# Kernel optimization log

Measured on AMD Instinct MI355X. Metric: run time of the kernel, lower is better.

## Reference

```python
import jax, jax.numpy as jnp
import numpy as np

EMB_K = 512
EMB_DIM = 256
BETA = 0.25
GAMMA = 0.99
EPS = 1e-5
B, T = 16, 4096


def setup_inputs() -> dict:
    key = jax.random.key(0)
    k1, k2, k3 = jax.random.split(key, 3)
    return {
        "inputs": jax.random.normal(k1, (B, EMB_DIM, T), dtype=jnp.float32),
        "emb_weight": jax.random.normal(k2, (EMB_K, EMB_DIM), dtype=jnp.float32),
        "ema_w": jax.random.normal(k3, (EMB_K, EMB_DIM), dtype=jnp.float32),
        "ema_cluster_size": jnp.zeros((EMB_K,), dtype=jnp.float32),
    }


def reference(inputs, emb_weight, ema_w, ema_cluster_size):
    # [B, D, T] -> [B, T, D]
    x = jnp.transpose(inputs, (0, 2, 1))
    flat = x.reshape(-1, EMB_DIM)  # [N, D]

    # squared euclidean distances to codebook: [N, K]
    dist = (jnp.sum(flat * flat, axis=1, keepdims=True)
            + jnp.sum(emb_weight * emb_weight, axis=1)
            - 2.0 * flat @ emb_weight.T)
    idx = jnp.argmin(dist, axis=1)            # [N]
    enc = jax.nn.one_hot(idx, EMB_K, dtype=flat.dtype)  # [N, K]

    # --- EMA codebook update (training branch) ---
    counts = jax.ops.segment_sum(jnp.ones_like(idx, dtype=flat.dtype), idx,
                                 num_segments=EMB_K)  # == enc.sum(0)
    new_cs = ema_cluster_size * GAMMA + (1.0 - GAMMA) * counts
    n = jnp.sum(new_cs)
    new_cs = (new_cs + EPS) / (n + EMB_K * EPS) * n
    dw = jax.ops.segment_sum(flat, idx, num_segments=EMB_K)  # == enc.T @ flat
    new_ema_w = ema_w * GAMMA + (1.0 - GAMMA) * dw
    new_emb_weight = new_ema_w / new_cs[:, None]

    # quantize with updated codebook (gather == enc @ new_emb_weight)
    Q = new_emb_weight[idx].reshape(x.shape)  # [B, T, D]

    e_latent_loss = jnp.mean((jax.lax.stop_gradient(Q) - x) ** 2)
    loss = BETA * e_latent_loss

    # straight-through
    Q_st = x + jax.lax.stop_gradient(Q - x)

    avg_probs = jnp.mean(enc, axis=0)
    PP = jnp.exp(-jnp.sum(avg_probs * jnp.log(avg_probs + 1e-10)))

    return loss, jnp.transpose(Q_st, (0, 2, 1)), PP, enc
```

## Files before the change

kernel.cpp:

```cpp
#include <hip/hip_runtime.h>

#define N_TOT 65536
#define DIM 256
#define KK 512
#define TT 4096
#define BB 16

typedef short bf16x8 __attribute__((ext_vector_type(8)));
typedef float f32x4 __attribute__((ext_vector_type(4)));

__device__ __forceinline__ ushort f2bf(float f) {
    unsigned u = __float_as_uint(f);
    unsigned r = (u + 0x7fffu + ((u >> 16) & 1u)) >> 16;
    return (ushort)r;
}

__global__ void k_se(const float* __restrict__ emb, float* __restrict__ se) {
    int wid = threadIdx.x >> 6, lane = threadIdx.x & 63;
    int k = blockIdx.x * 4 + wid;
    const float4* e4 = (const float4*)emb;
    float4 v = e4[k * 64 + lane];
    float s = v.x * v.x + v.y * v.y + v.z * v.z + v.w * v.w;
#pragma unroll
    for (int m = 1; m < 64; m <<= 1) s += __shfl_xor(s, m);
    if (lane == 0) se[k] = s;
}

__global__ void k_split_e(const float* __restrict__ emb, ushort* __restrict__ eb) {
    int k = blockIdx.x, tid = threadIdx.x;
    int c0 = tid * 4;
    float4 v = *(const float4*)(emb + k * DIM + c0);
    float f[4] = {v.x, v.y, v.z, v.w};
    ushort h[4], l[4];
#pragma unroll
    for (int j = 0; j < 4; ++j) {
        h[j] = f2bf(f[j]);
        float hf = __uint_as_float(((unsigned)h[j]) << 16);
        l[j] = f2bf(f[j] - hf);
    }
    uint2 hp = make_uint2((unsigned)h[0] | ((unsigned)h[1] << 16),
                          (unsigned)h[2] | ((unsigned)h[3] << 16));
    uint2 lp = make_uint2((unsigned)l[0] | ((unsigned)l[1] << 16),
                          (unsigned)l[2] | ((unsigned)l[3] << 16));
    *(uint2*)(eb + (size_t)k * 512 + c0) = hp;
    *(uint2*)(eb + (size_t)k * 512 + 256 + c0) = lp;
}

__global__ __launch_bounds__(256) void k_split_x(const float* __restrict__ in,
                                                 ushort* __restrict__ xt) {
    __shared__ float ls[64][65];
    int tid = threadIdx.x;
    int b = blockIdx.x >> 8;
    int rest = blockIdx.x & 255;
    int tt = rest >> 2, dt = rest & 3;
    int t0 = tt * 64, d0 = dt * 64;
    int tl = tid & 63, dg = tid >> 6;
    const float* src = in + (size_t)b * DIM * TT + t0 + tl;
#pragma unroll
    for (int p = 0; p < 16; ++p) {
        int d = dg * 16 + p;
        ls[d][tl] = src[(size_t)(d0 + d) * TT];
    }
    __syncthreads();
    int c0 = dg * 16;
    int n = b * TT + t0 + tl;
    ushort* row = xt + (size_t)n * 512;
    ushort h[16], l[16];
#pragma unroll
    for (int j = 0; j < 16; ++j) {
        float v = ls[c0 + j][tl];
        h[j] = f2bf(v);
        float hf = __uint_as_float(((unsigned)h[j]) << 16);
        l[j] = f2bf(v - hf);
    }
    uint hu[8], lu[8];
#pragma unroll
    for (int j = 0; j < 8; ++j) {
        hu[j] = (unsigned)h[2 * j] | ((unsigned)h[2 * j + 1] << 16);
        lu[j] = (unsigned)l[2 * j] | ((unsigned)l[2 * j + 1] << 16);
    }
    *(uint4*)(row + d0 + c0) = make_uint4(hu[0], hu[1], hu[2], hu[3]);
    *(uint4*)(row + d0 + c0 + 8) = make_uint4(hu[4], hu[5], hu[6], hu[7]);
    *(uint4*)(row + 256 + d0 + c0) = make_uint4(lu[0], lu[1], lu[2], lu[3]);
    *(uint4*)(row + 256 + d0 + c0 + 8) = make_uint4(lu[4], lu[5], lu[6], lu[7]);
}

__global__ void k_zero(float* __restrict__ dw, unsigned* __restrict__ counts,
                       unsigned* __restrict__ lossd) {
    int i = blockIdx.x * 256 + threadIdx.x;
    if (i < 131072) dw[i] = 0.f;
    int j = i - 131072;
    if (j >= 0 && j < 512) counts[j] = 0u;
    if (j >= 512 && j < 514) lossd[j - 512] = 0u;
}

__global__ __launch_bounds__(256) void k_dist(
    const ushort* __restrict__ xt, const ushort* __restrict__ eb,
    const float* __restrict__ se,
    float* __restrict__ partd, int* __restrict__ parti) {
    __shared__ ushort As[128 * 64];
    __shared__ ushort Bs[128 * 64];
    const int tid = threadIdx.x;
    const int lane = tid & 63, w = tid >> 6;
    const int bj = blockIdx.x, bi = blockIdx.y;
    const int n0 = bi * 128, k0 = bj * 128;
    const int wr = w >> 1, wc = w & 1;

    f32x4 acc[4][4] = {};

    for (int it = 0; it < 12; ++it) {
        const int region = it >> 2, sub = it & 3;
        const int aoff = (region == 2 ? 256 : 0) + sub * 64;
        const int boff = (region == 1 ? 256 : 0) + sub * 64;
#pragma unroll
        for (int i = 0; i < 4; ++i) {
            int r = i * 32 + w * 8 + (lane >> 3);
            int slot = (lane & 7) ^ (r & 7);
            const ushort* ga = xt + (size_t)(n0 + r) * 512 + aoff + slot * 8;
            const ushort* gb = eb + (size_t)(k0 + r) * 512 + boff + slot * 8;
            __builtin_amdgcn_global_load_lds(
                (const __attribute__((address_space(1))) void*)ga,
                (__attribute__((address_space(3))) void*)&As[(size_t)(i * 256 + w * 64) * 8],
                16, 0, 0);
            __builtin_amdgcn_global_load_lds(
                (const __attribute__((address_space(1))) void*)gb,
                (__attribute__((address_space(3))) void*)&Bs[(size_t)(i * 256 + w * 64) * 8],
                16, 0, 0);
        }
        __syncthreads();
#pragma unroll
        for (int kk = 0; kk < 2; ++kk) {
            bf16x8 af[4], bfr[4];
#pragma unroll
            for (int mi = 0; mi < 4; ++mi) {
                int row = wr * 64 + mi * 16 + (lane & 15);
                int slot = (kk * 4 + (lane >> 4)) ^ (row & 7);
                af[mi] = *(const bf16x8*)&As[row * 64 + slot * 8];
            }
#pragma unroll
            for (int ni = 0; ni < 4; ++ni) {
                int row = wc * 64 + ni * 16 + (lane & 15);
                int slot = (kk * 4 + (lane >> 4)) ^ (row & 7);
                bfr[ni] = *(const bf16x8*)&Bs[row * 64 + slot * 8];
            }
#pragma unroll
            for (int mi = 0; mi < 4; ++mi)
#pragma unroll
                for (int ni = 0; ni < 4; ++ni)
                    acc[mi][ni] = __builtin_amdgcn_mfma_f32_16x16x32_bf16(
                        af[mi], bfr[ni], acc[mi][ni], 0, 0, 0);
        }
        __syncthreads();
    }

    float* pd = (float*)As;
    int* pi = (int*)Bs;
#pragma unroll
    for (int mi = 0; mi < 4; ++mi) {
#pragma unroll
        for (int j = 0; j < 4; ++j) {
            int r = wr * 64 + mi * 16 + (lane >> 4) * 4 + j;
            float dmin = 3.4e38f;
            int bidx = 0x7fffffff;
#pragma unroll
            for (int ni = 0; ni < 4; ++ni) {
                int k = k0 + wc * 64 + ni * 16 + (lane & 15);
                float dv = fmaf(-2.f, acc[mi][ni][j], se[k]);
                if (dv < dmin) { dmin = dv; bidx = k; }
            }
            pd[r * 32 + wc * 16 + (lane & 15)] = dmin;
            pi[r * 32 + wc * 16 + (lane & 15)] = bidx;
        }
    }
    __syncthreads();
    if (tid < 128) {
        float dmin = 3.4e38f;
        int bidx = 0x7fffffff;
        for (int c = 0; c < 32; ++c) {
            float dv = pd[tid * 32 + c];
            int iv = pi[tid * 32 + c];
            if (dv < dmin || (dv == dmin && iv < bidx)) { dmin = dv; bidx = iv; }
        }
        partd[(size_t)bj * N_TOT + n0 + tid] = dmin;
        parti[(size_t)bj * N_TOT + n0 + tid] = bidx;
    }
}

__global__ void k_combine(const float* __restrict__ partd, const int* __restrict__ parti,
                          int* __restrict__ idx) {
    int n = blockIdx.x * 256 + threadIdx.x;
    float dmin = 3.4e38f;
    int bidx = 0x7fffffff;
#pragma unroll
    for (int p = 0; p < 4; ++p) {
        float dv = partd[(size_t)p * N_TOT + n];
        int iv = parti[(size_t)p * N_TOT + n];
        if (dv < dmin || (dv == dmin && iv < bidx)) { dmin = dv; bidx = iv; }
    }
    idx[n] = bidx;
}

__global__ void k_enc_zero(float2* __restrict__ enc2) {
    size_t base = (size_t)blockIdx.x * (256 * 32) + threadIdx.x;
#pragma unroll
    for (int j = 0; j < 32; ++j) enc2[base + j * 256] = make_float2(0.f, 0.f);
}

__global__ void k_enc_ones(const int* __restrict__ idx, float* __restrict__ enc) {
    int n = blockIdx.x * 256 + threadIdx.x;
    enc[(size_t)n * KK + idx[n]] = 1.0f;
}

__global__ void k_counts(const int* __restrict__ idx, unsigned* __restrict__ counts) {
    __shared__ unsigned h[512];
    int tid = threadIdx.x;
    h[tid] = 0u;
    h[tid + 256] = 0u;
    __syncthreads();
    int base = blockIdx.x * 1024;
    for (int n = base + tid; n < base + 1024; n += 256) atomicAdd(&h[idx[n]], 1u);
    __syncthreads();
    atomicAdd(&counts[tid], h[tid]);
    atomicAdd(&counts[tid + 256], h[tid + 256]);
}

__global__ void k_scalars(const unsigned* __restrict__ counts, const float* __restrict__ cs_in,
                          float* __restrict__ csn, float* __restrict__ pp_out) {
    __shared__ float red[512];
    int k = threadIdx.x;
    float c = (float)counts[k];
    float pre = cs_in[k] * 0.99f + 0.01f * c;
    red[k] = pre;
    __syncthreads();
#pragma unroll
    for (int s = 256; s > 0; s >>= 1) {
        if (k < s) red[k] += red[k + s];
        __syncthreads();
    }
    float nsum = red[0];
    __syncthreads();
    csn[k] = (pre + 1e-5f) / (nsum + 512 * 1e-5f) * nsum;
    float p = c * (1.0f / 65536.f);
    red[k] = -p * logf(p + 1e-10f);
    __syncthreads();
#pragma unroll
    for (int s = 256; s > 0; s >>= 1) {
        if (k < s) red[k] += red[k + s];
        __syncthreads();
    }
    if (k == 0) pp_out[0] = expf(red[0]);
}

__global__ __launch_bounds__(256) void k_dw(const float* __restrict__ in,
                                            const int* __restrict__ idx,
                                            float* __restrict__ dw) {
    __shared__ float hist[512][33];
    int tid = threadIdx.x;
    int b = blockIdx.x >> 3, d0 = (blockIdx.x & 7) * 32;
    for (int i = tid; i < 512 * 33; i += 256) (&hist[0][0])[i] = 0.f;
    __syncthreads();
    int w = tid >> 6, lane = tid & 63;
    const int* ip = idx + b * TT;
    const float* xb = in + (size_t)b * DIM * TT;
    for (int tc = 0; tc < 64; ++tc) {
        int t = tc * 64 + lane;
        int kk = ip[t];
#pragma unroll
        for (int dd = 0; dd < 8; ++dd) {
            int dl = w * 8 + dd;
            float v = xb[(size_t)(d0 + dl) * TT + t];
            atomicAdd(&hist[kk][dl], v);
        }
    }
    __syncthreads();
    for (int i = tid; i < 512 * 32; i += 256) {
        int k = i >> 5, dl = i & 31;
        atomicAdd(&dw[k * DIM + d0 + dl], hist[k][dl]);
    }
}

__global__ void k_newemb(const float* __restrict__ ema_w, const float* __restrict__ dw,
                         const float* __restrict__ csn, float* __restrict__ newemb) {
    int i = blockIdx.x * 256 + threadIdx.x;
    int k = i >> 8;
    newemb[i] = (ema_w[i] * 0.99f + 0.01f * dw[i]) / csn[k];
}

__global__ __launch_bounds__(256) void k_out1(const float* __restrict__ in,
                                              const int* __restrict__ idx,
                                              const float* __restrict__ newemb,
                                              float* __restrict__ out1,
                                              unsigned long long* __restrict__ lossd) {
    __shared__ float q[256][68];
    __shared__ float redl[4];
    int tid = threadIdx.x;
    int b = blockIdx.x >> 6, tc = blockIdx.x & 63;
    int tl = tid & 63, dg = tid >> 6;
    int kk = idx[b * TT + tc * 64 + tl];
    const float4* ne4 = (const float4*)(newemb + (size_t)kk * DIM);
#pragma unroll
    for (int d4 = 0; d4 < 16; ++d4) {
        float4 v = ne4[dg * 16 + d4];
        int d = dg * 64 + d4 * 4;
        q[d + 0][tl] = v.x;
        q[d + 1][tl] = v.y;
        q[d + 2][tl] = v.z;
        q[d + 3][tl] = v.w;
    }
    __syncthreads();
    float lacc = 0.f;
    const float* xb = in + (size_t)b * DIM * TT + tc * 64;
    float* ob = out1 + (size_t)b * DIM * TT + tc * 64;
#pragma unroll 4
    for (int j = 0; j < 64; ++j) {
        int fi = tid + 256 * j;
        int d = fi >> 6, t = fi & 63;
        float qv = q[d][t];
        float xv = xb[(size_t)d * TT + t];
        ob[(size_t)d * TT + t] = qv;
        float df = qv - xv;
        lacc = fmaf(df, df, lacc);
    }
#pragma unroll
    for (int m = 1; m < 64; m <<= 1) lacc += __shfl_xor(lacc, m);
    if ((tid & 63) == 0) redl[tid >> 6] = lacc;
    __syncthreads();
    if (tid == 0) {
        double s = (double)redl[0] + (double)redl[1] + (double)redl[2] + (double)redl[3];
        atomicAdd((double*)lossd, s);
    }
}

__global__ void k_loss_fin(const double* __restrict__ lossd, float* __restrict__ out0) {
    out0[0] = (float)(0.25 * lossd[0] * (1.0 / 16777216.0));
}

extern "C" void kernel_launch(void* const* d_in, const int* in_sizes, int n_in,
                              void* d_out, int out_size, void* d_ws, size_t ws_size,
                              hipStream_t stream) {
    const float* in = (const float*)d_in[0];
    const float* emb = (const float*)d_in[1];
    const float* emaw = (const float*)d_in[2];
    const float* cs = (const float*)d_in[3];
    float* out = (float*)d_out;
    char* ws = (char*)d_ws;

    float* se = (float*)(ws + 0);
    float* partd = (float*)(ws + 264192);
    int* parti = (int*)(ws + 1312768);
    int* idx = (int*)(ws + 2361344);
    unsigned* counts = (unsigned*)(ws + 2623488);
    float* csn = (float*)(ws + 2625536);
    float* dw = (float*)(ws + 2627584);
    float* newemb = (float*)(ws + 3151872);
    double* lossd = (double*)(ws + 3676160);
    ushort* eb = (ushort*)(ws + 3676416);
    ushort* xt = (ushort*)(ws + 4200704);

    float* out_loss = out;
    float* out_q = out + 1;
    float* out_pp = out + 16777217;
    float* enc = out + 16777218;

    hipLaunchKernelGGL(k_se, dim3(128), dim3(256), 0, stream, emb, se);
    hipLaunchKernelGGL(k_split_e, dim3(512), dim3(64), 0, stream, emb, eb);
    hipLaunchKernelGGL(k_split_x, dim3(4096), dim3(256), 0, stream, in, xt);
    hipLaunchKernelGGL(k_zero, dim3(515), dim3(256), 0, stream, dw, counts, (unsigned*)lossd);
    hipLaunchKernelGGL(k_dist, dim3(4, 512), dim3(256), 0, stream, xt, eb, se, partd, parti);
    hipLaunchKernelGGL(k_combine, dim3(256), dim3(256), 0, stream, partd, parti, idx);
    hipLaunchKernelGGL(k_enc_zero, dim3(2048), dim3(256), 0, stream, (float2*)enc);
    hipLaunchKernelGGL(k_enc_ones, dim3(256), dim3(256), 0, stream, idx, enc);
    hipLaunchKernelGGL(k_counts, dim3(64), dim3(256), 0, stream, idx, counts);
    hipLaunchKernelGGL(k_scalars, dim3(1), dim3(512), 0, stream, counts, cs, csn, out_pp);
    hipLaunchKernelGGL(k_dw, dim3(128), dim3(256), 0, stream, in, idx, dw);
    hipLaunchKernelGGL(k_newemb, dim3(512), dim3(256), 0, stream, emaw, dw, csn, newemb);
    hipLaunchKernelGGL(k_out1, dim3(1024), dim3(256), 0, stream, in, idx, newemb, out_q,
                       (unsigned long long*)lossd);
    hipLaunchKernelGGL(k_loss_fin, dim3(1), dim3(1), 0, stream, lossd, out_loss);
}
```

Baseline: 391.8 us.

## Replace LDS-atomic dw histogram with counting-sort gather and per-cluster reduction

A prefix scan is added to k_scalars to give per-cluster offsets. A new scatter kernel then bucket-sorts token indices by their assigned code. The dw accumulation now reads the pre-split hi/lo bf16 rows for each cluster's tokens and sums them in registers, adding the two halves with a shuffle and issuing few global atomics; this replaces the 128-block kernel that did heavy LDS atomics over strided fp32 input. The enc zero-fill kernel is also replaced with hipMemsetAsync. The cost is an extra launch plus global atomics in the scatter, and load imbalance across clusters of very different size.

Measured after the change: 444.0 us. 1.13x slower.

```diff
diff --git a/kernel.cpp b/kernel.cpp
--- a/kernel.cpp
+++ b/kernel.cpp
@@ -200,12 +200,6 @@
     idx[n] = bidx;
 }
 
-__global__ void k_enc_zero(float2* __restrict__ enc2) {
-    size_t base = (size_t)blockIdx.x * (256 * 32) + threadIdx.x;
-#pragma unroll
-    for (int j = 0; j < 32; ++j) enc2[base + j * 256] = make_float2(0.f, 0.f);
-}
-
 __global__ void k_enc_ones(const int* __restrict__ idx, float* __restrict__ enc) {
     int n = blockIdx.x * 256 + threadIdx.x;
     enc[(size_t)n * KK + idx[n]] = 1.0f;
@@ -225,12 +219,16 @@
 }
 
 __global__ void k_scalars(const unsigned* __restrict__ counts, const float* __restrict__ cs_in,
-                          float* __restrict__ csn, float* __restrict__ pp_out) {
+                          float* __restrict__ csn, float* __restrict__ pp_out,
+                          unsigned* __restrict__ offs, unsigned* __restrict__ cursor) {
     __shared__ float red[512];
+    __shared__ unsigned sc[512];
     int k = threadIdx.x;
-    float c = (float)counts[k];
+    unsigned ci = counts[k];
+    float c = (float)ci;
     float pre = cs_in[k] * 0.99f + 0.01f * c;
     red[k] = pre;
+    sc[k] = ci;
     __syncthreads();
 #pragma unroll
     for (int s = 256; s > 0; s >>= 1) {
@@ -249,33 +247,50 @@
         __syncthreads();
     }
     if (k == 0) pp_out[0] = expf(red[0]);
-}
-
-__global__ __launch_bounds__(256) void k_dw(const float* __restrict__ in,
-                                            const int* __restrict__ idx,
-                                            float* __restrict__ dw) {
-    __shared__ float hist[512][33];
-    int tid = threadIdx.x;
-    int b = blockIdx.x >> 3, d0 = (blockIdx.x & 7) * 32;
-    for (int i = tid; i < 512 * 33; i += 256) (&hist[0][0])[i] = 0.f;
-    __syncthreads();
-    int w = tid >> 6, lane = tid & 63;
-    const int* ip = idx + b * TT;
-    const float* xb = in + (size_t)b * DIM * TT;
-    for (int tc = 0; tc < 64; ++tc) {
-        int t = tc * 64 + lane;
-        int kk = ip[t];
-#pragma unroll
-        for (int dd = 0; dd < 8; ++dd) {
-            int dl = w * 8 + dd;
-            float v = xb[(size_t)(d0 + dl) * TT + t];
-            atomicAdd(&hist[kk][dl], v);
+#pragma unroll
+    for (int s = 1; s < 512; s <<= 1) {
+        unsigned v = (k >= s) ? sc[k - s] : 0u;
+        __syncthreads();
+        sc[k] += v;
+        __syncthreads();
+    }
+    unsigned excl = sc[k] - ci;
+    offs[k] = excl;
+    cursor[k] = excl;
+}
+
+__global__ void k_scatter(const int* __restrict__ idx, unsigned* __restrict__ cursor,
+                          int* __restrict__ sorted) {
+    int n = blockIdx.x * 256 + threadIdx.x;
+    int k = idx[n];
+    unsigned p = atomicAdd(&cursor[k], 1u);
+    sorted[p] = n;
+}
+
+__global__ __launch_bounds__(64) void k_dwsum(const ushort* __restrict__ xt,
+                                              const int* __restrict__ sorted,
+                                              const unsigned* __restrict__ offs,
+                                              const unsigned* __restrict__ counts,
+                                              float* __restrict__ dw) {
+    int k = blockIdx.x >> 4, c = blockIdx.x & 15;
+    int lane = threadIdx.x;
+    unsigned beg = offs[k], cnt = counts[k];
+    float acc[8] = {0.f, 0.f, 0.f, 0.f, 0.f, 0.f, 0.f, 0.f};
+    for (unsigned i = c; i < cnt; i += 16) {
+        int n = sorted[beg + i];
+        uint4 v = *(const uint4*)(xt + (size_t)n * 512 + lane * 8);
+        unsigned u[4] = {v.x, v.y, v.z, v.w};
+#pragma unroll
+        for (int j = 0; j < 4; ++j) {
+            acc[2 * j] += __uint_as_float(u[j] << 16);
+            acc[2 * j + 1] += __uint_as_float(u[j] & 0xffff0000u);
         }
     }
-    __syncthreads();
-    for (int i = tid; i < 512 * 32; i += 256) {
-        int k = i >> 5, dl = i & 31;
-        atomicAdd(&dw[k * DIM + d0 + dl], hist[k][dl]);
+#pragma unroll
+    for (int j = 0; j < 8; ++j) {
+        float other = __shfl(acc[j], lane + 32);
+        if (lane < 32 && (acc[j] != 0.f || other != 0.f))
+            atomicAdd(&dw[k * DIM + lane * 8 + j], acc[j] + other);
     }
 }
 
@@ -356,6 +371,9 @@
     double* lossd = (double*)(ws + 3676160);
     ushort* eb = (ushort*)(ws + 3676416);
     ushort* xt = (ushort*)(ws + 4200704);
+    int* sorted = (int*)(ws + 71309568);
+    unsigned* offs = (unsigned*)(ws + 71571712);
+    unsigned* cursor = (unsigned*)(ws + 71573760);
 
     float* out_loss = out;
     float* out_q = out + 1;
@@ -368,11 +386,13 @@
     hipLaunchKernelGGL(k_zero, dim3(515), dim3(256), 0, stream, dw, counts, (unsigned*)lossd);
     hipLaunchKernelGGL(k_dist, dim3(4, 512), dim3(256), 0, stream, xt, eb, se, partd, parti);
     hipLaunchKernelGGL(k_combine, dim3(256), dim3(256), 0, stream, partd, parti, idx);
-    hipLaunchKernelGGL(k_enc_zero, dim3(2048), dim3(256), 0, stream, (float2*)enc);
+    hipMemsetAsync(enc, 0, (size_t)N_TOT * KK * sizeof(float), stream);
     hipLaunchKernelGGL(k_enc_ones, dim3(256), dim3(256), 0, stream, idx, enc);
     hipLaunchKernelGGL(k_counts, dim3(64), dim3(256), 0, stream, idx, counts);
-    hipLaunchKernelGGL(k_scalars, dim3(1), dim3(512), 0, stream, counts, cs, csn, out_pp);
-    hipLaunchKernelGGL(k_dw, dim3(128), dim3(256), 0, stream, in, idx, dw);
+    hipLaunchKernelGGL(k_scalars, dim3(1), dim3(512), 0, stream, counts, cs, csn, out_pp,
+                       offs, cursor);
+    hipLaunchKernelGGL(k_scatter, dim3(256), dim3(256), 0, stream, idx, cursor, sorted);
+    hipLaunchKernelGGL(k_dwsum, dim3(8192), dim3(64), 0, stream, xt, sorted, offs, counts, dw);
     hipLaunchKernelGGL(k_newemb, dim3(512), dim3(256), 0, stream, emaw, dw, csn, newemb);
     hipLaunchKernelGGL(k_out1, dim3(1024), dim3(256), 0, stream, in, idx, newemb, out_q,
                        (unsigned long long*)lossd);
```
